# Kernel tuning notes

Measured on AMD Instinct MI355X. Metric: run time of the kernel, lower is better.

Reference implementation:

```python
import jax, jax.numpy as jnp
import numpy as np

N_ATOMS = 200000
N_BONDS = 400000
MAX_NB = 6
HID = 128
ATOM_FDIM = 151
BOND_FDIM = 165
N_HEADS = 2


def _layer_norm(x, g, b, eps=1e-5):
    mu = jnp.mean(x, axis=-1, keepdims=True)
    var = jnp.var(x, axis=-1, keepdims=True)
    return g * (x - mu) * jax.lax.rsqrt(var + eps) + b


def setup_inputs() -> dict:
    key = jax.random.key(0)
    ks = jax.random.split(key, 12)
    s = 0.05  # weight init scale
    return {
        'f_atoms': jax.random.normal(ks[0], (N_ATOMS, ATOM_FDIM), jnp.float32),
        'f_bonds': jax.random.normal(ks[1], (N_BONDS, BOND_FDIM), jnp.float32),
        'a2a': jax.random.randint(ks[2], (N_ATOMS, MAX_NB), 0, N_ATOMS, jnp.int32),
        'a2b': jax.random.randint(ks[3], (N_ATOMS, MAX_NB), 0, N_BONDS, jnp.int32),
        'W_i': jax.random.normal(ks[4], (ATOM_FDIM, HID), jnp.float32) * s,
        'b_i': jnp.zeros((HID,), jnp.float32),
        'ln1_g': jnp.ones((HID,), jnp.float32),
        'ln1_b': jnp.zeros((HID,), jnp.float32),
        'Wh_q': jax.random.normal(ks[5], (N_HEADS, HID + BOND_FDIM, HID), jnp.float32) * s,
        'bh_q': jnp.zeros((N_HEADS, HID), jnp.float32),
        'Wh_k': jax.random.normal(ks[6], (N_HEADS, HID + BOND_FDIM, HID), jnp.float32) * s,
        'bh_k': jnp.zeros((N_HEADS, HID), jnp.float32),
        'Wh_v': jax.random.normal(ks[7], (N_HEADS, HID + BOND_FDIM, HID), jnp.float32) * s,
        'bh_v': jnp.zeros((N_HEADS, HID), jnp.float32),
        'W_o': jax.random.normal(ks[8], (N_HEADS * HID, HID), jnp.float32) * s,
        'b_o': jnp.zeros((HID,), jnp.float32),
        'ln2_g': jnp.ones((HID,), jnp.float32),
        'ln2_b': jnp.zeros((HID,), jnp.float32),
    }


def reference(f_atoms, f_bonds, a2a, a2b, W_i, b_i, ln1_g, ln1_b,
              Wh_q, bh_q, Wh_k, bh_k, Wh_v, bh_v, W_o, b_o, ln2_g, ln2_b):
    # Input projection of raw atom features: dropout(layernorm(act(W_i x)))
    # (dropout = identity in eval).
    h0 = _layer_norm(jax.nn.relu(f_atoms @ W_i + b_i), ln1_g, ln1_b)  # [N, H]

    # Graph gather: neighbor atom hidden states + incident bond raw features.
    nei_a = h0[a2a]       # [N, nb, H]   irregular gather
    nei_b = f_bonds[a2b]  # [N, nb, Fb]  irregular gather
    # Aggregate messages once; shared across Q/K/V branches and heads.
    msg = jnp.concatenate([nei_a, nei_b], axis=-1).sum(axis=1)  # [N, H+Fb]

    def branch(Wh, bh):  # Wh: [heads, H+Fb, H] -> [N, heads, H]
        return jax.nn.relu(h0[:, None, :] + jnp.einsum('nf,efh->neh', msg, Wh) + bh)

    Q = branch(Wh_q, bh_q)  # [N, heads, H]
    K = branch(Wh_k, bh_k)
    V = branch(Wh_v, bh_v)

    # Attention across the heads axis (per atom).
    scores = jnp.einsum('nqh,nkh->nqk', Q, K) / jnp.sqrt(jnp.float32(HID))
    attn = jax.nn.softmax(scores, axis=-1)
    x = jnp.einsum('nqk,nkh->nqh', attn, V).reshape(Q.shape[0], -1)  # [N, heads*H]

    x_out = x @ W_o + b_o  # [N, H]
    # Residual sublayer connection.
    f_atoms_out = h0 + _layer_norm(x_out, ln2_g, ln2_b)
    return f_atoms_out
```

## Files before the change

### kernel.cpp

```cpp
#include <hip/hip_runtime.h>

typedef unsigned short u16;
typedef unsigned int u32;
typedef __attribute__((ext_vector_type(8))) short s8v;
typedef __attribute__((ext_vector_type(4))) float f4v;
typedef __attribute__((ext_vector_type(2))) float f2v;

#define NATOMS 200000
#define NBONDS 400000

__device__ __forceinline__ float b2f(u32 u) {
    union { u32 i; float f; } v; v.i = u << 16; return v.f;
}
__device__ __forceinline__ u16 f2b(float f) {
    union { float f; u32 i; } v; v.f = f;
    u32 r = v.i + 0x7fffu + ((v.i >> 16) & 1u);
    return (u16)(r >> 16);
}
__device__ __forceinline__ uint4 pack8(const float* f) {
    uint4 o;
    o.x = (u32)f2b(f[0]) | ((u32)f2b(f[1]) << 16);
    o.y = (u32)f2b(f[2]) | ((u32)f2b(f[3]) << 16);
    o.z = (u32)f2b(f[4]) | ((u32)f2b(f[5]) << 16);
    o.w = (u32)f2b(f[6]) | ((u32)f2b(f[7]) << 16);
    return o;
}
__device__ __forceinline__ void acc8(uint4 u, float* a) {
    a[0] += b2f(u.x & 0xffffu); a[1] += b2f(u.x >> 16);
    a[2] += b2f(u.y & 0xffffu); a[3] += b2f(u.y >> 16);
    a[4] += b2f(u.z & 0xffffu); a[5] += b2f(u.z >> 16);
    a[6] += b2f(u.w & 0xffffu); a[7] += b2f(u.w >> 16);
}

__global__ void k_wprep(const float* __restrict__ Whq, const float* __restrict__ Whk,
                        const float* __restrict__ Whv, const float* __restrict__ Wo,
                        const float* __restrict__ Wi,
                        u16* __restrict__ wallw, u16* __restrict__ wow, u16* __restrict__ wiw) {
    int t = blockIdx.x * 256 + threadIdx.x;
    if (t < 245760) {
        int ks = t / 24576, rem = t % 24576;
        int n = rem >> 5, kk = rem & 31;
        int k = ks * 32 + kk;
        int hg = n / 48, r48 = n % 48;
        int branch = r48 >> 4, r16i = r48 & 15;
        int head = r16i >> 3, h = hg * 8 + (r16i & 7);
        const float* Wp = (branch == 0) ? Whq : ((branch == 1) ? Whk : Whv);
        float val = (k < 293) ? Wp[(head * 293 + k) * 128 + h] : 0.f;
        wallw[t] = f2b(val);
    } else if (t < 278528) {
        int u = t - 245760;
        int ks = u >> 12, n = (u >> 5) & 127, kk = u & 31;
        int k = ks * 32 + kk;
        wow[u] = f2b(Wo[k * 128 + n]);
    } else if (t < 299008) {
        int u = t - 278528;
        int ks = u >> 12, n = (u >> 5) & 127, kk = u & 31;
        int k = ks * 32 + kk;
        wiw[u] = (k < 151) ? f2b(Wi[k * 128 + n]) : (u16)0;
    }
}

__global__ void k_bond16(const float* __restrict__ fb, u16* __restrict__ fbw) {
    int t = blockIdx.x * 256 + threadIdx.x;
    if (t >= NBONDS * 21) return;
    u32 b = (u32)t / 21u, c = (u32)t % 21u;
    const float* src = fb + (size_t)b * 165 + c * 8;
    float a[8];
    #pragma unroll
    for (int q = 0; q < 8; q++) a[q] = ((int)(c * 8 + q) < 165) ? src[q] : 0.f;
    *(uint4*)&fbw[(size_t)b * 168 + c * 8] = pack8(a);
}

__global__ void k_msgb(const u16* __restrict__ fbw, const int* __restrict__ a2b,
                       u16* __restrict__ msgb) {
    int t = blockIdx.x * 256 + threadIdx.x;
    if (t >= NATOMS * 21) return;
    u32 atom = (u32)t / 21u, c = (u32)t % 21u;
    const int* nb = a2b + (size_t)atom * 6;
    float a[8] = {0, 0, 0, 0, 0, 0, 0, 0};
    #pragma unroll
    for (int j = 0; j < 6; j++)
        acc8(*(const uint4*)&fbw[(size_t)(u32)nb[j] * 168 + c * 8], a);
    *(uint4*)&msgb[(size_t)atom * 168 + c * 8] = pack8(a);
}

__global__ void k_msga(const u16* __restrict__ h0w, const int* __restrict__ a2a,
                       u16* __restrict__ msga) {
    int t = blockIdx.x * 256 + threadIdx.x;
    if (t >= NATOMS * 16) return;
    u32 atom = (u32)t >> 4, c = (u32)t & 15u;
    const int* na = a2a + (size_t)atom * 6;
    float a[8] = {0, 0, 0, 0, 0, 0, 0, 0};
    #pragma unroll
    for (int j = 0; j < 6; j++)
        acc8(*(const uint4*)&h0w[(size_t)(u32)na[j] * 128 + c * 8], a);
    *(uint4*)&msga[(size_t)atom * 128 + c * 8] = pack8(a);
}

#define H0_SMEM (64 * 168 * 2 + 64 * 132 * 4)
__global__ __launch_bounds__(256) void k_h0(
    const float* __restrict__ fa, const u16* __restrict__ wiw,
    const float* __restrict__ bi, const float* __restrict__ g1, const float* __restrict__ b1,
    u16* __restrict__ h0w) {
    extern __shared__ char smem[];
    u16* la = (u16*)smem;
    float* lo = (float*)(smem + 21504);
    const int tid = threadIdx.x;
    const size_t abase = (size_t)blockIdx.x * 64;

    for (int i = tid; i < 64 * 151; i += 256) {
        int r = i / 151, c = i - r * 151;
        la[r * 168 + c] = f2b(fa[(abase + r) * 151 + c]);
    }
    for (int i = tid; i < 64 * 17; i += 256) {
        int r = i / 17, c = i - r * 17;
        la[r * 168 + 151 + c] = 0;
    }
    __syncthreads();

    const int w = tid >> 6, l = tid & 63;
    const int r16 = l & 15, kq = l >> 4;
    f4v acc[4][2];
    #pragma unroll
    for (int m = 0; m < 4; m++)
        #pragma unroll
        for (int c = 0; c < 2; c++)
            #pragma unroll
            for (int v = 0; v < 4; v++) acc[m][c][v] = 0.f;

    #pragma unroll
    for (int ks = 0; ks < 5; ++ks) {
        s8v af[4];
        #pragma unroll
        for (int m = 0; m < 4; m++)
            af[m] = *(const s8v*)&la[(m * 16 + r16) * 168 + ks * 32 + kq * 8];
        #pragma unroll
        for (int c = 0; c < 2; c++) {
            int n = w * 32 + c * 16 + r16;
            s8v bf = *(const s8v*)&wiw[ks * 4096 + n * 32 + kq * 8];
            #pragma unroll
            for (int m = 0; m < 4; m++)
                acc[m][c] = __builtin_amdgcn_mfma_f32_16x16x32_bf16(af[m], bf, acc[m][c], 0, 0, 0);
        }
    }
    #pragma unroll
    for (int c = 0; c < 2; c++) {
        int col = w * 32 + c * 16 + r16;
        float bias = bi[col];
        #pragma unroll
        for (int m = 0; m < 4; m++) {
            #pragma unroll
            for (int v = 0; v < 4; v++) {
                int row = m * 16 + kq * 4 + v;
                lo[row * 132 + col] = fmaxf(acc[m][c][v] + bias, 0.f);
            }
        }
    }
    __syncthreads();

    const int ga = tid >> 2, sb = tid & 3;
    float vals[32], s = 0.f, s2 = 0.f;
    #pragma unroll
    for (int j = 0; j < 32; j++) {
        float v = lo[ga * 132 + sb + 4 * j];
        vals[j] = v; s += v; s2 += v * v;
    }
    s += __shfl_xor(s, 1); s += __shfl_xor(s, 2);
    s2 += __shfl_xor(s2, 1); s2 += __shfl_xor(s2, 2);
    float mu = s * (1.f / 128.f), var = s2 * (1.f / 128.f) - mu * mu;
    float rs = rsqrtf(var + 1e-5f);
    u16* orow = h0w + (abase + ga) * 128;
    #pragma unroll
    for (int j = 0; j < 32; j++) {
        int col = sb + 4 * j;
        orow[col] = f2b(g1[col] * (vals[j] - mu) * rs + b1[col]);
    }
}

#define SMEM_FUSED 73728
__global__ __launch_bounds__(1024) void k_fused(
    const u16* __restrict__ h0w, const u16* __restrict__ msga, const u16* __restrict__ msgb,
    const u16* __restrict__ wallw, const u16* __restrict__ wow,
    const float* __restrict__ bhq, const float* __restrict__ bhk, const float* __restrict__ bhv,
    const float* __restrict__ bo, const float* __restrict__ g2, const float* __restrict__ b2,
    float* __restrict__ out) {
    extern __shared__ char smem[];
    u16* lx = (u16*)smem;
    float* attn = (float*)(smem + 33792);
    float* pp = (float*)(smem + 34816);
    u16* lh0 = (u16*)(smem + 40960);
    float* sco2 = (float*)(smem + 57344);

    const int tid = threadIdx.x;
    const size_t abase = (size_t)blockIdx.x * 64;
    const int w = tid >> 6, l = tid & 63;
    const int r16 = l & 15, kq = l >> 4;
    const u32 xmask = (u32)((r16 & 7) << 4);

    const u16* bp = wallw + (size_t)(w * 48 + r16) * 32 + kq * 8;
    s8v bfA0 = *(const s8v*)&bp[0];
    s8v bfA1 = *(const s8v*)&bp[512];
    s8v bfA2 = *(const s8v*)&bp[1024];

    {
        int r = tid >> 4, cc = (tid & 15) << 3;
        *(uint4*)&lh0[r * 128 + cc] = *(const uint4*)&h0w[(abase + r) * 128 + cc];
    }

    #pragma unroll
    for (int ii = 0; ii < 3; ++ii) {
        int i = tid + ii * 1024;
        if (i < 2560) {
            int r = i / 40, c = i - r * 40;
            uint4 val;
            if (c < 16) {
                val = *(const uint4*)&msga[(abase + r) * 128 + c * 8];
            } else if (c < 37) {
                val = *(const uint4*)&msgb[(abase + r) * 168 + (c - 16) * 8];
            } else {
                val = (uint4){0, 0, 0, 0};
            }
            *(uint4*)(smem + (((u32)(r * 640 + c * 16)) ^ ((u32)((r & 7) << 4)))) = val;
        }
    }
    __syncthreads();

    f4v acc[4][3];
    #pragma unroll
    for (int m = 0; m < 4; m++)
        #pragma unroll
        for (int c = 0; c < 3; c++)
            #pragma unroll
            for (int v = 0; v < 4; v++) acc[m][c][v] = 0.f;

    s8v bfB0, bfB1, bfB2;
    #pragma unroll
    for (int kp = 0; kp < 5; ++kp) {
        {
            const int ks = 2 * kp;
            const u16* nb = bp + (size_t)(ks + 1) * 24576;
            bfB0 = *(const s8v*)&nb[0];
            bfB1 = *(const s8v*)&nb[512];
            bfB2 = *(const s8v*)&nb[1024];
            #pragma unroll
            for (int m = 0; m < 4; m++) {
                s8v af = *(const s8v*)(smem +
                    (((u32)((m * 16 + r16) * 640 + ks * 64 + kq * 16)) ^ xmask));
                acc[m][0] = __builtin_amdgcn_mfma_f32_16x16x32_bf16(af, bfA0, acc[m][0], 0, 0, 0);
                acc[m][1] = __builtin_amdgcn_mfma_f32_16x16x32_bf16(af, bfA1, acc[m][1], 0, 0, 0);
                acc[m][2] = __builtin_amdgcn_mfma_f32_16x16x32_bf16(af, bfA2, acc[m][2], 0, 0, 0);
            }
        }
        {
            const int ks = 2 * kp + 1;
            if (kp < 4) {
                const u16* nb = bp + (size_t)(ks + 1) * 24576;
                bfA0 = *(const s8v*)&nb[0];
                bfA1 = *(const s8v*)&nb[512];
                bfA2 = *(const s8v*)&nb[1024];
            }
            #pragma unroll
            for (int m = 0; m < 4; m++) {
                s8v af = *(const s8v*)(smem +
                    (((u32)((m * 16 + r16) * 640 + ks * 64 + kq * 16)) ^ xmask));
                acc[m][0] = __builtin_amdgcn_mfma_f32_16x16x32_bf16(af, bfB0, acc[m][0], 0, 0, 0);
                acc[m][1] = __builtin_amdgcn_mfma_f32_16x16x32_bf16(af, bfB1, acc[m][1], 0, 0, 0);
                acc[m][2] = __builtin_amdgcn_mfma_f32_16x16x32_bf16(af, bfB2, acc[m][2], 0, 0, 0);
            }
        }
    }

    const int head = r16 >> 3;
    const int h = w * 8 + (r16 & 7);
    const float bq = bhq[head * 128 + h];
    const float bk = bhk[head * 128 + h];
    const float bv = bhv[head * 128 + h];
    #pragma unroll
    for (int m = 0; m < 4; m++) {
        #pragma unroll
        for (int v = 0; v < 4; v++) {
            int row = m * 16 + kq * 4 + v;
            float h0v = b2f(lh0[row * 128 + h]);
            float q  = fmaxf(acc[m][0][v] + h0v + bq, 0.f);
            float kk = fmaxf(acc[m][1][v] + h0v + bk, 0.f);
            float vv = fmaxf(acc[m][2][v] + h0v + bv, 0.f);
            acc[m][2][v] = vv;
            float kx = __shfl_xor(kk, 8);
            float pA = q * kk;
            float pB = q * kx;
            pA += __shfl_xor(pA, 1); pA += __shfl_xor(pA, 2); pA += __shfl_xor(pA, 4);
            pB += __shfl_xor(pB, 1); pB += __shfl_xor(pB, 2); pB += __shfl_xor(pB, 4);
            if ((r16 & 7) == ((m * 4 + v) & 7)) {
                f2v pr; pr[0] = pA; pr[1] = pB;
                *(f2v*)&sco2[(w * 64 + row) * 4 + head * 2] = pr;
            }
        }
    }
    __syncthreads();

    if (tid < 128) {
        int atom = tid >> 1, qh = tid & 1;
        float ss = 0.f, sx = 0.f;
        #pragma unroll
        for (int ww = 0; ww < 16; ww++) {
            f2v p = *(const f2v*)&sco2[(ww * 64 + atom) * 4 + qh * 2];
            ss += p[0]; sx += p[1];
        }
        const float sc = 0.08838834764831845f;
        ss *= sc; sx *= sc;
        float mm = fmaxf(ss, sx);
        float e0 = __expf(ss - mm), e1 = __expf(sx - mm);
        float inv = 1.f / (e0 + e1);
        attn[atom * 4 + qh * 2] = e0 * inv;
        attn[atom * 4 + qh * 2 + 1] = e1 * inv;
    }
    __syncthreads();

    #pragma unroll
    for (int m = 0; m < 4; m++) {
        #pragma unroll
        for (int v = 0; v < 4; v++) {
            int row = m * 16 + kq * 4 + v;
            f2v a = *(const f2v*)&attn[row * 4 + head * 2];
            float vv = acc[m][2][v];
            float vx = __shfl_xor(vv, 8);
            lx[row * 264 + head * 128 + h] = f2b(a[0] * vv + a[1] * vx);
        }
    }
    __syncthreads();

    const int mb = w >> 2, ch = w & 3;
    f4v oa0, oa1;
    #pragma unroll
    for (int v = 0; v < 4; v++) { oa0[v] = 0.f; oa1[v] = 0.f; }
    const u16* xp = lx + (mb * 16 + r16) * 264 + kq * 8;
    const u16* wp2 = wow + (ch * 32 + r16) * 32 + kq * 8;
    #pragma unroll
    for (int ks = 0; ks < 8; ks++) {
        s8v a = *(const s8v*)&xp[ks * 32];
        s8v b0 = *(const s8v*)&wp2[ks * 4096];
        s8v b1 = *(const s8v*)&wp2[ks * 4096 + 512];
        oa0 = __builtin_amdgcn_mfma_f32_16x16x32_bf16(a, b0, oa0, 0, 0, 0);
        oa1 = __builtin_amdgcn_mfma_f32_16x16x32_bf16(a, b1, oa1, 0, 0, 0);
    }

    const int col0 = ch * 32 + r16, col1 = col0 + 16;
    const float bo0 = bo[col0], bo1 = bo[col1];
    float xo0[4], xo1[4], sv[4], s2v[4];
    #pragma unroll
    for (int v = 0; v < 4; v++) {
        xo0[v] = oa0[v] + bo0;
        xo1[v] = oa1[v] + bo1;
        float s = xo0[v] + xo1[v];
        float s2 = xo0[v] * xo0[v] + xo1[v] * xo1[v];
        s += __shfl_xor(s, 1); s += __shfl_xor(s, 2);
        s += __shfl_xor(s, 4); s += __shfl_xor(s, 8);
        s2 += __shfl_xor(s2, 1); s2 += __shfl_xor(s2, 2);
        s2 += __shfl_xor(s2, 4); s2 += __shfl_xor(s2, 8);
        sv[v] = s; s2v[v] = s2;
    }
    if (r16 == 0) {
        #pragma unroll
        for (int v = 0; v < 4; v++) {
            int row = mb * 16 + kq * 4 + v;
            pp[row * 8 + ch * 2] = sv[v];
            pp[row * 8 + ch * 2 + 1] = s2v[v];
        }
    }
    __syncthreads();

    const float ga0 = g2[col0], ga1 = g2[col1];
    const float bb0 = b2[col0], bb1 = b2[col1];
    #pragma unroll
    for (int v = 0; v < 4; v++) {
        int row = mb * 16 + kq * 4 + v;
        f4v p0 = *(f4v*)&pp[row * 8];
        f4v p1 = *(f4v*)&pp[row * 8 + 4];
        float ssum = p0[0] + p0[2] + p1[0] + p1[2];
        float s2sum = p0[1] + p0[3] + p1[1] + p1[3];
        float mu = ssum * (1.f / 128.f);
        float var = s2sum * (1.f / 128.f) - mu * mu;
        float rs = rsqrtf(var + 1e-5f);
        float* orow = out + (abase + row) * 128;
        orow[col0] = ga0 * (xo0[v] - mu) * rs + bb0 + b2f(lh0[row * 128 + col0]);
        orow[col1] = ga1 * (xo1[v] - mu) * rs + bb1 + b2f(lh0[row * 128 + col1]);
    }
}

extern "C" void kernel_launch(void* const* d_in, const int* in_sizes, int n_in,
                              void* d_out, int out_size, void* d_ws, size_t ws_size,
                              hipStream_t stream) {
    const float* f_atoms = (const float*)d_in[0];
    const float* f_bonds = (const float*)d_in[1];
    const int* a2a = (const int*)d_in[2];
    const int* a2b = (const int*)d_in[3];
    const float* W_i = (const float*)d_in[4];
    const float* b_i = (const float*)d_in[5];
    const float* ln1g = (const float*)d_in[6];
    const float* ln1b = (const float*)d_in[7];
    const float* Whq = (const float*)d_in[8];
    const float* bhq = (const float*)d_in[9];
    const float* Whk = (const float*)d_in[10];
    const float* bhk = (const float*)d_in[11];
    const float* Whv = (const float*)d_in[12];
    const float* bhv = (const float*)d_in[13];
    const float* Wo = (const float*)d_in[14];
    const float* bo = (const float*)d_in[15];
    const float* ln2g = (const float*)d_in[16];
    const float* ln2b = (const float*)d_in[17];
    float* out = (float*)d_out;

    char* ws = (char*)d_ws;
    u16* h0w = (u16*)(ws + 0);
    u16* fbw = (u16*)(ws + 51200000);
    u16* msga = (u16*)(ws + 51200000);
    u16* msgb = (u16*)(ws + 185600000);
    u16* wallw = (u16*)(ws + 252800000);
    u16* wow = (u16*)(ws + 253291520);
    u16* wiw = (u16*)(ws + 253357056);

    hipFuncSetAttribute(reinterpret_cast<const void*>(k_fused),
                        hipFuncAttributeMaxDynamicSharedMemorySize, SMEM_FUSED);

    k_wprep<<<1168, 256, 0, stream>>>(Whq, Whk, Whv, Wo, W_i, wallw, wow, wiw);
    k_bond16<<<32813, 256, 0, stream>>>(f_bonds, fbw);
    k_h0<<<3125, 256, H0_SMEM, stream>>>(f_atoms, wiw, b_i, ln1g, ln1b, h0w);
    k_msgb<<<16407, 256, 0, stream>>>(fbw, a2b, msgb);
    k_msga<<<12500, 256, 0, stream>>>(h0w, a2a, msga);
    k_fused<<<3125, 1024, SMEM_FUSED, stream>>>(h0w, msga, msgb, wallw, wow,
                                                bhq, bhk, bhv, bo, ln2g, ln2b, out);
}
```

Baseline: 607.5 us.

## Halve atoms per block in fused kernel, shrink LDS, use DPP reductions

The fused attention kernel now handles 32 atoms per block instead of 64, launches twice as many blocks, reuses the staging buffer for score partials, pads the h0 tile, and cuts LDS from 72KB to about 29KB so more blocks can be resident per CU. Cross-lane reductions move from shfl_xor to DPP and ds_swizzle, and the output projection gives each wave one 16-column MFMA tile instead of two. The cost is that every block reloads the full per-wave B-fragment weights for half as many atoms, plus an extra barrier.

```diff
diff --git a/kernel.cpp b/kernel.cpp
--- a/kernel.cpp
+++ b/kernel.cpp
@@ -30,6 +30,28 @@
     a[2] += b2f(u.y & 0xffffu); a[3] += b2f(u.y >> 16);
     a[4] += b2f(u.z & 0xffffu); a[5] += b2f(u.z >> 16);
     a[6] += b2f(u.w & 0xffffu); a[7] += b2f(u.w >> 16);
+}
+
+template<int C>
+__device__ __forceinline__ float dpp_mov_f(float x) {
+    return __int_as_float(__builtin_amdgcn_update_dpp(
+        0, __float_as_int(x), C, 0xF, 0xF, true));
+}
+__device__ __forceinline__ float swz_xor4(float x) {
+    return __int_as_float(__builtin_amdgcn_ds_swizzle(__float_as_int(x), 0x101F));
+}
+__device__ __forceinline__ float red8(float x) {
+    x += dpp_mov_f<0xB1>(x);
+    x += dpp_mov_f<0x4E>(x);
+    x += swz_xor4(x);
+    return x;
+}
+__device__ __forceinline__ float red16(float x) {
+    x += dpp_mov_f<0xB1>(x);
+    x += dpp_mov_f<0x4E>(x);
+    x += swz_xor4(x);
+    x += dpp_mov_f<0x128>(x);
+    return x;
 }
 
 __global__ void k_wprep(const float* __restrict__ Whq, const float* __restrict__ Whk,
@@ -177,22 +199,22 @@
     }
 }
 
-#define SMEM_FUSED 73728
-__global__ __launch_bounds__(1024) void k_fused(
+#define SMEM_FUSED 29184
+__global__ __launch_bounds__(1024, 8) void k_fused(
     const u16* __restrict__ h0w, const u16* __restrict__ msga, const u16* __restrict__ msgb,
     const u16* __restrict__ wallw, const u16* __restrict__ wow,
     const float* __restrict__ bhq, const float* __restrict__ bhk, const float* __restrict__ bhv,
     const float* __restrict__ bo, const float* __restrict__ g2, const float* __restrict__ b2,
     float* __restrict__ out) {
     extern __shared__ char smem[];
+    float* sco2 = (float*)smem;
     u16* lx = (u16*)smem;
-    float* attn = (float*)(smem + 33792);
-    float* pp = (float*)(smem + 34816);
-    u16* lh0 = (u16*)(smem + 40960);
-    float* sco2 = (float*)(smem + 57344);
+    float* attn = (float*)(smem + 16896);
+    float* pp = (float*)(smem + 17408);
+    u16* lh0 = (u16*)(smem + 20480);
 
     const int tid = threadIdx.x;
-    const size_t abase = (size_t)blockIdx.x * 64;
+    const size_t abase = (size_t)blockIdx.x * 32;
     const int w = tid >> 6, l = tid & 63;
     const int r16 = l & 15, kq = l >> 4;
     const u32 xmask = (u32)((r16 & 7) << 4);
@@ -202,15 +224,15 @@
     s8v bfA1 = *(const s8v*)&bp[512];
     s8v bfA2 = *(const s8v*)&bp[1024];
 
-    {
-        int r = tid >> 4, cc = (tid & 15) << 3;
-        *(uint4*)&lh0[r * 128 + cc] = *(const uint4*)&h0w[(abase + r) * 128 + cc];
-    }
-
-    #pragma unroll
-    for (int ii = 0; ii < 3; ++ii) {
+    if (tid < 512) {
+        int r = tid >> 4, c8 = tid & 15;
+        *(uint4*)&lh0[r * 136 + c8 * 8] = *(const uint4*)&h0w[(abase + r) * 128 + c8 * 8];
+    }
+
+    #pragma unroll
+    for (int ii = 0; ii < 2; ++ii) {
         int i = tid + ii * 1024;
-        if (i < 2560) {
+        if (i < 1280) {
             int r = i / 40, c = i - r * 40;
             uint4 val;
             if (c < 16) {
@@ -225,9 +247,9 @@
     }
     __syncthreads();
 
-    f4v acc[4][3];
-    #pragma unroll
-    for (int m = 0; m < 4; m++)
+    f4v acc[2][3];
+    #pragma unroll
+    for (int m = 0; m < 2; m++)
         #pragma unroll
         for (int c = 0; c < 3; c++)
             #pragma unroll
@@ -243,7 +265,7 @@
             bfB1 = *(const s8v*)&nb[512];
             bfB2 = *(const s8v*)&nb[1024];
             #pragma unroll
-            for (int m = 0; m < 4; m++) {
+            for (int m = 0; m < 2; m++) {
                 s8v af = *(const s8v*)(smem +
                     (((u32)((m * 16 + r16) * 640 + ks * 64 + kq * 16)) ^ xmask));
                 acc[m][0] = __builtin_amdgcn_mfma_f32_16x16x32_bf16(af, bfA0, acc[m][0], 0, 0, 0);
@@ -260,7 +282,7 @@
                 bfA2 = *(const s8v*)&nb[1024];
             }
             #pragma unroll
-            for (int m = 0; m < 4; m++) {
+            for (int m = 0; m < 2; m++) {
                 s8v af = *(const s8v*)(smem +
                     (((u32)((m * 16 + r16) * 640 + ks * 64 + kq * 16)) ^ xmask));
                 acc[m][0] = __builtin_amdgcn_mfma_f32_16x16x32_bf16(af, bfB0, acc[m][0], 0, 0, 0);
@@ -269,6 +291,7 @@
             }
         }
     }
+    __syncthreads();
 
     const int head = r16 >> 3;
     const int h = w * 8 + (r16 & 7);
@@ -276,34 +299,32 @@
     const float bk = bhk[head * 128 + h];
     const float bv = bhv[head * 128 + h];
     #pragma unroll
-    for (int m = 0; m < 4; m++) {
+    for (int m = 0; m < 2; m++) {
         #pragma unroll
         for (int v = 0; v < 4; v++) {
             int row = m * 16 + kq * 4 + v;
-            float h0v = b2f(lh0[row * 128 + h]);
+            float h0v = b2f(lh0[row * 136 + h]);
             float q  = fmaxf(acc[m][0][v] + h0v + bq, 0.f);
             float kk = fmaxf(acc[m][1][v] + h0v + bk, 0.f);
             float vv = fmaxf(acc[m][2][v] + h0v + bv, 0.f);
             acc[m][2][v] = vv;
-            float kx = __shfl_xor(kk, 8);
-            float pA = q * kk;
-            float pB = q * kx;
-            pA += __shfl_xor(pA, 1); pA += __shfl_xor(pA, 2); pA += __shfl_xor(pA, 4);
-            pB += __shfl_xor(pB, 1); pB += __shfl_xor(pB, 2); pB += __shfl_xor(pB, 4);
-            if ((r16 & 7) == ((m * 4 + v) & 7)) {
+            float kx = dpp_mov_f<0x128>(kk);
+            float pA = red8(q * kk);
+            float pB = red8(q * kx);
+            if ((r16 & 7) == (m * 4 + v)) {
                 f2v pr; pr[0] = pA; pr[1] = pB;
-                *(f2v*)&sco2[(w * 64 + row) * 4 + head * 2] = pr;
-            }
-        }
-    }
-    __syncthreads();
-
-    if (tid < 128) {
+                *(f2v*)&sco2[(w * 32 + row) * 4 + head * 2] = pr;
+            }
+        }
+    }
+    __syncthreads();
+
+    if (tid < 64) {
         int atom = tid >> 1, qh = tid & 1;
         float ss = 0.f, sx = 0.f;
         #pragma unroll
         for (int ww = 0; ww < 16; ww++) {
-            f2v p = *(const f2v*)&sco2[(ww * 64 + atom) * 4 + qh * 2];
+            f2v p = *(const f2v*)&sco2[(ww * 32 + atom) * 4 + qh * 2];
             ss += p[0]; sx += p[1];
         }
         const float sc = 0.08838834764831845f;
@@ -317,73 +338,62 @@
     __syncthreads();
 
     #pragma unroll
-    for (int m = 0; m < 4; m++) {
+    for (int m = 0; m < 2; m++) {
         #pragma unroll
         for (int v = 0; v < 4; v++) {
             int row = m * 16 + kq * 4 + v;
             f2v a = *(const f2v*)&attn[row * 4 + head * 2];
             float vv = acc[m][2][v];
-            float vx = __shfl_xor(vv, 8);
+            float vx = dpp_mov_f<0x128>(vv);
             lx[row * 264 + head * 128 + h] = f2b(a[0] * vv + a[1] * vx);
         }
     }
     __syncthreads();
 
-    const int mb = w >> 2, ch = w & 3;
-    f4v oa0, oa1;
-    #pragma unroll
-    for (int v = 0; v < 4; v++) { oa0[v] = 0.f; oa1[v] = 0.f; }
+    const int mb = w >> 3, ch = w & 7;
+    f4v oa;
+    #pragma unroll
+    for (int v = 0; v < 4; v++) oa[v] = 0.f;
     const u16* xp = lx + (mb * 16 + r16) * 264 + kq * 8;
-    const u16* wp2 = wow + (ch * 32 + r16) * 32 + kq * 8;
+    const u16* wp2 = wow + (ch * 16 + r16) * 32 + kq * 8;
     #pragma unroll
     for (int ks = 0; ks < 8; ks++) {
         s8v a = *(const s8v*)&xp[ks * 32];
-        s8v b0 = *(const s8v*)&wp2[ks * 4096];
-        s8v b1 = *(const s8v*)&wp2[ks * 4096 + 512];
-        oa0 = __builtin_amdgcn_mfma_f32_16x16x32_bf16(a, b0, oa0, 0, 0, 0);
-        oa1 = __builtin_amdgcn_mfma_f32_16x16x32_bf16(a, b1, oa1, 0, 0, 0);
-    }
-
-    const int col0 = ch * 32 + r16, col1 = col0 + 16;
-    const float bo0 = bo[col0], bo1 = bo[col1];
-    float xo0[4], xo1[4], sv[4], s2v[4];
+        s8v b = *(const s8v*)&wp2[ks * 4096];
+        oa = __builtin_amdgcn_mfma_f32_16x16x32_bf16(a, b, oa, 0, 0, 0);
+    }
+
+    const int col = ch * 16 + r16;
+    const float boc = bo[col];
+    float xo[4];
     #pragma unroll
     for (int v = 0; v < 4; v++) {
-        xo0[v] = oa0[v] + bo0;
-        xo1[v] = oa1[v] + bo1;
-        float s = xo0[v] + xo1[v];
-        float s2 = xo0[v] * xo0[v] + xo1[v] * xo1[v];
-        s += __shfl_xor(s, 1); s += __shfl_xor(s, 2);
-        s += __shfl_xor(s, 4); s += __shfl_xor(s, 8);
-        s2 += __shfl_xor(s2, 1); s2 += __shfl_xor(s2, 2);
-        s2 += __shfl_xor(s2, 4); s2 += __shfl_xor(s2, 8);
-        sv[v] = s; s2v[v] = s2;
-    }
-    if (r16 == 0) {
-        #pragma unroll
-        for (int v = 0; v < 4; v++) {
+        xo[v] = oa[v] + boc;
+        float s = red16(xo[v]);
+        float s2 = red16(xo[v] * xo[v]);
+        if (r16 == 0) {
             int row = mb * 16 + kq * 4 + v;
-            pp[row * 8 + ch * 2] = sv[v];
-            pp[row * 8 + ch * 2 + 1] = s2v[v];
-        }
-    }
-    __syncthreads();
-
-    const float ga0 = g2[col0], ga1 = g2[col1];
-    const float bb0 = b2[col0], bb1 = b2[col1];
+            f2v pr; pr[0] = s; pr[1] = s2;
+            *(f2v*)&pp[(row * 8 + ch) * 2] = pr;
+        }
+    }
+    __syncthreads();
+
+    const float gac = g2[col], bbc = b2[col];
     #pragma unroll
     for (int v = 0; v < 4; v++) {
         int row = mb * 16 + kq * 4 + v;
-        f4v p0 = *(f4v*)&pp[row * 8];
-        f4v p1 = *(f4v*)&pp[row * 8 + 4];
-        float ssum = p0[0] + p0[2] + p1[0] + p1[2];
-        float s2sum = p0[1] + p0[3] + p1[1] + p1[3];
+        f4v p0 = *(f4v*)&pp[row * 16];
+        f4v p1 = *(f4v*)&pp[row * 16 + 4];
+        f4v p2 = *(f4v*)&pp[row * 16 + 8];
+        f4v p3 = *(f4v*)&pp[row * 16 + 12];
+        float ssum = p0[0] + p0[2] + p1[0] + p1[2] + p2[0] + p2[2] + p3[0] + p3[2];
+        float s2sum = p0[1] + p0[3] + p1[1] + p1[3] + p2[1] + p2[3] + p3[1] + p3[3];
         float mu = ssum * (1.f / 128.f);
         float var = s2sum * (1.f / 128.f) - mu * mu;
         float rs = rsqrtf(var + 1e-5f);
-        float* orow = out + (abase + row) * 128;
-        orow[col0] = ga0 * (xo0[v] - mu) * rs + bb0 + b2f(lh0[row * 128 + col0]);
-        orow[col1] = ga1 * (xo1[v] - mu) * rs + bb1 + b2f(lh0[row * 128 + col1]);
+        out[(abase + row) * 128 + col] =
+            gac * (xo[v] - mu) * rs + bbc + b2f(lh0[row * 136 + col]);
     }
 }
 
@@ -427,6 +437,6 @@
     k_h0<<<3125, 256, H0_SMEM, stream>>>(f_atoms, wiw, b_i, ln1g, ln1b, h0w);
     k_msgb<<<16407, 256, 0, stream>>>(fbw, a2b, msgb);
     k_msga<<<12500, 256, 0, stream>>>(h0w, a2a, msga);
-    k_fused<<<3125, 1024, SMEM_FUSED, stream>>>(h0w, msga, msgb, wallw, wow,
+    k_fused<<<6250, 1024, SMEM_FUSED, stream>>>(h0w, msga, msgb, wallw, wow,
                                                 bhq, bhk, bhv, bo, ln2g, ln2b, out);
 }
```

Result: faster. 564.0 us (-7.2%).
